# Kernel optimization log

Hardware: AMD Instinct MI355X
Metric: run time of the kernel (lower is better)

The kernel has to match this reference:

```python
import jax, jax.numpy as jnp
import numpy as np

D_INPUT, D_MODEL, D_OUTPUT, D_STATE, FACTOR = 100, 256, 100, 64, 2
N2 = D_STATE // 2  # complex conjugate-pair states (S4D)
B_SZ, L_SEQ = 16, 4096


def setup_inputs() -> dict:
    key = jax.random.key(0)
    ks = jax.random.split(key, 12)
    H, N = D_MODEL, N2
    # S4D ('diag-lin', zoh, real_transform='exp') parameters
    log_dt = jax.random.uniform(ks[0], (H,)) * (np.log(0.1) - np.log(0.001)) + np.log(0.001)
    log_A_real = jnp.log(0.5 * jnp.ones((H, N), jnp.float32))
    A_imag = jnp.pi * jnp.broadcast_to(jnp.arange(N, dtype=jnp.float32), (H, N))
    B_re = jnp.ones((H, N), jnp.float32)
    B_im = jnp.zeros((H, N), jnp.float32)
    C_re = jax.random.normal(ks[1], (H, N), jnp.float32)
    C_im = jax.random.normal(ks[2], (H, N), jnp.float32)
    Dskip = jax.random.normal(ks[3], (H,), jnp.float32)
    return {
        'x': jax.random.normal(ks[4], (B_SZ, L_SEQ, D_INPUT), jnp.float32),
        'enc_w': jax.random.normal(ks[5], (D_MODEL, D_INPUT), jnp.float32) / np.sqrt(D_INPUT),
        'enc_b': jnp.zeros((D_MODEL,), jnp.float32),
        'log_dt': log_dt, 'log_A_real': log_A_real, 'A_imag': A_imag,
        'B_re': B_re, 'B_im': B_im, 'C_re': C_re, 'C_im': C_im, 'Dskip': Dskip,
        'ln_g': jnp.ones((D_MODEL,), jnp.float32),
        'ln_b': jnp.zeros((D_MODEL,), jnp.float32),
        'dec1_w': jax.random.normal(ks[6], (D_MODEL * FACTOR, D_MODEL), jnp.float32) / np.sqrt(D_MODEL),
        'dec1_b': jnp.zeros((D_MODEL * FACTOR,), jnp.float32),
        'dec2_w': jax.random.normal(ks[7], (D_OUTPUT, D_MODEL * FACTOR), jnp.float32) / np.sqrt(D_MODEL * FACTOR),
        'dec2_b': jnp.zeros((D_OUTPUT,), jnp.float32),
    }


def s4d_kernel(log_dt, log_A_real, A_imag, B_re, B_im, C_re, C_im, L):
    # diagonal SSM kernel, ZOH discretization: K[h,l] = 2 Re sum_n C'_hn exp(dt_h A_hn)^l
    dt = jnp.exp(log_dt)[:, None]                      # (H,1)
    A = -jnp.exp(log_A_real) + 1j * A_imag             # (H,N)
    C = (B_re + 1j * B_im) * (C_re + 1j * C_im)        # (H,N), B folded into C
    dtA = dt * A                                       # (H,N)
    C = C * (jnp.exp(dtA) - 1.0) / A                   # ZOH correction
    V = jnp.exp(dtA[:, :, None] * jnp.arange(L))       # (H,N,L) Vandermonde
    return 2.0 * jnp.einsum('hn,hnl->hl', C, V).real   # (H,L)


def reference(x, enc_w, enc_b, log_dt, log_A_real, A_imag, B_re, B_im, C_re, C_im,
              Dskip, ln_g, ln_b, dec1_w, dec1_b, dec2_w, dec2_b):
    B, L, _ = x.shape
    u = (x @ enc_w.T + enc_b).transpose(0, 2, 1)       # (B,H,L)
    # FFTConv (single layer), dropout = identity (eval)
    k = s4d_kernel(log_dt, log_A_real, A_imag, B_re, B_im, C_re, C_im, L)
    n = 2 * L
    y = jnp.fft.irfft(jnp.fft.rfft(u, n=n) * jnp.fft.rfft(k, n=n)[None], n=n)[..., :L]
    y = y + u * Dskip[None, :, None]
    y = jax.nn.gelu(y, approximate=False)
    h = y + u                                          # residual
    # LayerNorm over channel dim
    t = h.transpose(0, 2, 1)                           # (B,L,H)
    mu = t.mean(-1, keepdims=True)
    var = jnp.mean((t - mu) ** 2, axis=-1, keepdims=True)
    t = (t - mu) / jnp.sqrt(var + 1e-5) * ln_g + ln_b
    # decoder MLP
    out = jax.nn.gelu(t @ dec1_w.T + dec1_b, approximate=False) @ dec2_w.T + dec2_b
    return out
```

## Files before the change

kernel.cpp:

```cpp
#include <hip/hip_runtime.h>
#include <hip/hip_bf16.h>

#define BB    16
#define LL    4096
#define DIN   100
#define HD    256
#define NN    32
#define DHID  512
#define DOUT  100
#define MROWS (BB*LL)
#define CH    64
#define CC    64
#define NCH   (BB*CC)

#define OFF_WRE    0
#define OFF_WIM    8192
#define OFF_KRE    16384
#define OFF_KIM    24576
#define OFF_WCHR   32768
#define OFF_WCHI   40960
#define OFF_ENCB   49152
#define OFF_DSK    49408
#define OFF_LNG    49664
#define OFF_LNB    49920
#define OFF_B1     50176
#define OFF_B2     50688
#define OFF_WENCB  50816
#define OFF_W1B    67200
#define OFF_W2B    132736
#define OFF_WFL    165504
#define OFF_BY     1230464
#define OFF_VST    2279040
#define OFF_UH     2803328
#define OFF_S      11191936
#define OFF_YH     19580544
#define OFF_TB     OFF_S
#define OFF_G0     OFF_UH
#define OFF_G1     OFF_YH
#define OFF_XB     OFF_YH

typedef __bf16 bf16x8 __attribute__((ext_vector_type(8)));
typedef float  f32x4  __attribute__((ext_vector_type(4)));

static __device__ __forceinline__ int probe_bf16(const void* lng) {
    return ((const unsigned int*)lng)[0] != 0x3f800000u;
}
static __device__ __forceinline__ float ldin(const void* p, long i, int isbf) {
    return isbf ? __bfloat162float(((const __hip_bfloat16*)p)[i]) : ((const float*)p)[i];
}
static __device__ __forceinline__ unsigned short f2bf(float v) {
    union { float f; unsigned u; } c; c.f = v;
    unsigned r = c.u + 0x7fffu + ((c.u >> 16) & 1u);
    return (unsigned short)(r >> 16);
}
static __device__ __forceinline__ float bf2f(unsigned short v) {
    union { unsigned u; float f; } c; c.u = ((unsigned)v) << 16; return c.f;
}
static __device__ __forceinline__ float gelu_f(float x) {
    float z  = fabsf(x) * 0.70710678118654752f;
    float tt = __builtin_amdgcn_rcpf(fmaf(0.3275911f, z, 1.0f));
    float p  = tt * fmaf(tt, fmaf(tt, fmaf(tt, fmaf(tt, 1.061405429f, -1.453152027f),
                          1.421413741f), -0.284496736f), 0.254829592f);
    float er = 1.0f - p * __expf(-z * z);
    return 0.5f * x * (1.0f + copysignf(er, x));
}
static __device__ __forceinline__ void gl2lds16(const unsigned short* g, unsigned short* l) {
    __builtin_amdgcn_global_load_lds(
        (const __attribute__((address_space(1))) unsigned int*)g,
        (__attribute__((address_space(3))) unsigned int*)l, 16, 0, 0);
}

__global__ __launch_bounds__(256) void k_prep(
    const void* encw, const void* encb, const void* logdt, const void* loga,
    const void* aim, const void* bre, const void* bim, const void* cre,
    const void* cim, const void* dsk, const void* lng, const void* lnb,
    const void* w1, const void* b1, const void* w2, const void* b2, float* ws)
{
    const int isbf = probe_bf16(lng);
    unsigned short* WEB = (unsigned short*)(ws + OFF_WENCB);
    unsigned short* W1B = (unsigned short*)(ws + OFF_W1B);
    unsigned short* W2B = (unsigned short*)(ws + OFF_W2B);
    const int total = 8192 + 256*4 + 512 + 128 + 32768 + 131072 + 65536;
    for (int idx = blockIdx.x * blockDim.x + threadIdx.x; idx < total;
         idx += gridDim.x * blockDim.x) {
        int i = idx;
        if (i < 8192) {
            int h = i >> 5;
            float dt  = expf(ldin(logdt, h, isbf));
            float Are = -expf(ldin(loga, i, isbf));
            float Aim = ldin(aim, i, isbf);
            float er  = expf(dt * Are);
            float sv, cv; sincosf(dt * Aim, &sv, &cv);
            float wre = er * cv, wim = er * sv;
            float Bre = ldin(bre, i, isbf), Bim = ldin(bim, i, isbf);
            float Cre = ldin(cre, i, isbf), Cim = ldin(cim, i, isbf);
            float C0re = Bre*Cre - Bim*Cim;
            float C0im = Bre*Cim + Bim*Cre;
            float inv = 1.0f / (Are*Are + Aim*Aim);
            float nre = wre - 1.0f, nim = wim;
            float Zre = (nre*Are + nim*Aim) * inv;
            float Zim = (nim*Are - nre*Aim) * inv;
            float kre = 2.0f * (C0re*Zre - C0im*Zim);
            float kim = -2.0f * (C0re*Zim + C0im*Zre);
            ws[OFF_WRE + i] = wre;  ws[OFF_WIM + i] = wim;
            ws[OFF_KRE + i] = kre;  ws[OFF_KIM + i] = kim;
            float* Wf = ws + OFF_WFL + (long)h * 4160 + 2*(i & 31);
            float pr = 1.0f, pi = 0.0f;
            for (int d = 0; d <= 64; ++d) {
                Wf[d*64]     = pr;
                Wf[d*64 + 1] = pi;
                float tr = pr*wre - pi*wim;
                pi = pr*wim + pi*wre; pr = tr;
            }
            ws[OFF_WCHR + i] = Wf[64*64];
            ws[OFF_WCHI + i] = Wf[64*64 + 1];
        } else if ((i -= 8192) < 256) {
            ws[OFF_ENCB + i] = ldin(encb, i, isbf);
        } else if ((i -= 256) < 256) {
            ws[OFF_DSK + i] = ldin(dsk, i, isbf);
        } else if ((i -= 256) < 256) {
            ws[OFF_LNG + i] = ldin(lng, i, isbf);
        } else if ((i -= 256) < 256) {
            ws[OFF_LNB + i] = ldin(lnb, i, isbf);
        } else if ((i -= 256) < 512) {
            ws[OFF_B1 + i] = ldin(b1, i, isbf);
        } else if ((i -= 512) < 128) {
            ws[OFF_B2 + i] = (i < 100) ? ldin(b2, i, isbf) : 0.0f;
        } else if ((i -= 128) < 32768) {
            int h = i >> 7, k = i & 127;
            WEB[i] = (k < 100) ? f2bf(ldin(encw, (long)h*100 + k, isbf)) : (unsigned short)0;
        } else if ((i -= 32768) < 131072) {
            W1B[i] = f2bf(ldin(w1, i, isbf));
        } else if ((i -= 131072) < 65536) {
            int j = i >> 9, k = i & 511;
            W2B[i] = (j < 100) ? f2bf(ldin(w2, (long)j*512 + k, isbf)) : (unsigned short)0;
        }
    }
}

__global__ __launch_bounds__(256) void k_xcvt(const void* x, const void* lng, float* ws)
{
    const int isbf = probe_bf16(lng);
    unsigned short* Xb = (unsigned short*)(ws + OFF_XB);
    const int total = 65536 * 16;
    for (int s = blockIdx.x * 256 + threadIdx.x; s < total; s += 1024 * 256) {
        int row = s >> 4, slot = s & 15;
        int k0 = slot * 8;
        unsigned short pk[8];
        if (!isbf) {
            const float* xr = (const float*)x + (long)row * 100;
            if (slot < 12) {
                float4 a = *(const float4*)(xr + k0);
                float4 b = *(const float4*)(xr + k0 + 4);
                pk[0]=f2bf(a.x); pk[1]=f2bf(a.y); pk[2]=f2bf(a.z); pk[3]=f2bf(a.w);
                pk[4]=f2bf(b.x); pk[5]=f2bf(b.y); pk[6]=f2bf(b.z); pk[7]=f2bf(b.w);
            } else if (slot == 12) {
                float4 a = *(const float4*)(xr + 96);
                pk[0]=f2bf(a.x); pk[1]=f2bf(a.y); pk[2]=f2bf(a.z); pk[3]=f2bf(a.w);
                pk[4]=0; pk[5]=0; pk[6]=0; pk[7]=0;
            } else {
                #pragma unroll
                for (int j = 0; j < 8; ++j) pk[j] = 0;
            }
        } else {
            const unsigned short* xr = (const unsigned short*)x + (long)row * 100;
            if (slot < 12) {
                *(uint2*)&pk[0] = *(const uint2*)(xr + k0);
                *(uint2*)&pk[4] = *(const uint2*)(xr + k0 + 4);
            } else if (slot == 12) {
                *(uint2*)&pk[0] = *(const uint2*)(xr + 96);
                pk[4]=0; pk[5]=0; pk[6]=0; pk[7]=0;
            } else {
                #pragma unroll
                for (int j = 0; j < 8; ++j) pk[j] = 0;
            }
        }
        *(float4*)&Xb[(long)row * 128 + k0] = *(const float4*)pk;
    }
}

__global__ __launch_bounds__(256) void k_tker(float* ws)
{
    __shared__ float Wp[65*65];
    __shared__ float kr[32], ki[32], Ks[64];
    int h = blockIdx.x;
    int t = threadIdx.x;
    for (int idx = t; idx < 4160; idx += 256) {
        int d = idx >> 6, c = idx & 63;
        Wp[d*65 + c] = ws[OFF_WFL + (long)h*4160 + idx];
    }
    if (t < 32) kr[t] = ws[OFF_KRE + h*32 + t];
    else if (t < 64) ki[t-32] = ws[OFF_KIM + h*32 + (t-32)];
    __syncthreads();
    if (t < 64) {
        float s = 0.0f;
        #pragma unroll
        for (int n = 0; n < 32; ++n)
            s += kr[n]*Wp[t*65 + 2*n] + ki[n]*Wp[t*65 + 2*n + 1];
        Ks[t] = s;
    }
    __syncthreads();
    unsigned short* BY = (unsigned short*)(ws + OFF_BY) + (long)h*8192;
    for (int idx = t; idx < 8192; idx += 256) {
        int j = idx >> 7, k = idx & 127;
        float v;
        if (k < 64) {
            v = (k <= j) ? Ks[j - k] : 0.0f;
        } else {
            int c = k - 64, n = c >> 1;
            float pr = Wp[(j+1)*65 + 2*n], pi = Wp[(j+1)*65 + 2*n + 1];
            v = ((c & 1) == 0) ? (kr[n]*pr + ki[n]*pi) : (ki[n]*pr - kr[n]*pi);
        }
        BY[idx] = f2bf(v);
    }
    unsigned short* Vst = (unsigned short*)(ws + OFF_VST) + (long)h*4096;
    for (int idx = t; idx < 4096; idx += 256) {
        int comp = idx >> 6, i = idx & 63;
        Vst[idx] = f2bf(Wp[(63 - i)*65 + comp]);
    }
}

__global__ __launch_bounds__(256) void k_encm(float* ws)
{
    __shared__ unsigned short SM[32768];
    unsigned short* Cs = SM;
    const unsigned short* Xb  = (const unsigned short*)(ws + OFF_XB);
    const unsigned short* WEB = (const unsigned short*)(ws + OFF_WENCB);
    int bid = blockIdx.x;
    int rt = bid >> 1, ct = bid & 1;
    long row0 = (long)rt * 128;
    int c0 = ct * 128;
    int t = threadIdx.x;
    int lane = t & 63, wv = t >> 6;
    int wm = (wv & 1) * 64, wn = (wv >> 1) * 64;
    int quad = lane >> 4, mr = lane & 15;
    int swz = lane & 7;
    int sr = t >> 3, sdst = (t & 7) * 8, ssrc = ((t & 7) ^ (sr & 7)) * 8;
    f32x4 acc[4][4] = {};
    #pragma unroll
    for (int it = 0; it < 4; ++it) {
        int r = sr + it * 32;
        gl2lds16(&Xb[(row0 + r) * 128 + ssrc], &SM[r * 64 + sdst]);
        gl2lds16(&WEB[(long)(c0 + r) * 128 + ssrc], &SM[8192 + r * 64 + sdst]);
    }
    __syncthreads();
    #pragma unroll
    for (int kc = 0; kc < 2; ++kc) {
        const unsigned short* As = &SM[(kc & 1) * 16384];
        const unsigned short* Bs = As + 8192;
        if (kc == 0) {
            #pragma unroll
            for (int it = 0; it < 4; ++it) {
                int r = sr + it * 32;
                gl2lds16(&Xb[(row0 + r) * 128 + 64 + ssrc], &SM[16384 + r * 64 + sdst]);
                gl2lds16(&WEB[(long)(c0 + r) * 128 + 64 + ssrc], &SM[24576 + r * 64 + sdst]);
            }
        }
        #pragma unroll
        for (int ks = 0; ks < 64; ks += 32) {
            int co = (((ks >> 3) | quad) ^ swz) * 8;
            bf16x8 af[4], bfr[4];
            #pragma unroll
            for (int i = 0; i < 4; ++i)
                af[i] = *(const bf16x8*)&As[(wm + i*16 + mr)*64 + co];
            #pragma unroll
            for (int j = 0; j < 4; ++j)
                bfr[j] = *(const bf16x8*)&Bs[(wn + j*16 + mr)*64 + co];
            #pragma unroll
            for (int i = 0; i < 4; ++i)
                #pragma unroll
                for (int j = 0; j < 4; ++j)
                    acc[i][j] = __builtin_amdgcn_mfma_f32_16x16x32_bf16(af[i], bfr[j], acc[i][j], 0, 0, 0);
        }
        __syncthreads();
    }
    const float* eb = ws + OFF_ENCB;
    #pragma unroll
    for (int j = 0; j < 4; ++j) {
        int hloc = wn + j*16 + mr;
        float bb = eb[c0 + hloc];
        #pragma unroll
        for (int i = 0; i < 4; ++i) {
            int l0 = wm + i*16 + quad*4;
            unsigned short pk[4];
            #pragma unroll
            for (int reg = 0; reg < 4; ++reg)
                pk[reg] = f2bf(acc[i][j][reg] + bb);
            *(uint2*)&Cs[hloc*136 + l0] = *(uint2*)pk;
        }
    }
    __syncthreads();
    unsigned short* Uh = (unsigned short*)(ws + OFF_UH);
    #pragma unroll
    for (int it = 0; it < 8; ++it) {
        int idx = t + it*256;
        int hh = idx >> 4, f = idx & 15;
        *(float4*)&Uh[(long)(c0 + hh)*65536 + row0 + f*8] = *(const float4*)&Cs[hh*136 + f*8];
    }
}

__global__ __launch_bounds__(256) void k_state(float* ws)
{
    __shared__ unsigned short As[128][72];
    __shared__ unsigned short Bs[64][72];
    const unsigned short* Uh  = (const unsigned short*)(ws + OFF_UH);
    const unsigned short* Vst = (const unsigned short*)(ws + OFF_VST);
    int bid = blockIdx.x;
    int h = bid >> 3, ct = bid & 7;
    int c0r = ct * 128;
    int t = threadIdx.x;
    int lane = t & 63, wv = t >> 6;
    int wm = (wv & 1) * 64, wn = (wv >> 1) * 32;
    int quad = lane >> 4, mr = lane & 15;
    const unsigned short* Ubase = Uh + (long)h * 65536;
    #pragma unroll
    for (int it = 0; it < 4; ++it) {
        int idx = t + it*256;
        int r = idx >> 3, f = idx & 7;
        *(float4*)&As[r][f*8] = *(const float4*)&Ubase[(long)(c0r + r)*64 + f*8];
    }
    #pragma unroll
    for (int it = 0; it < 2; ++it) {
        int idx = t + it*256;
        int r = idx >> 3, f = idx & 7;
        *(float4*)&Bs[r][f*8] = *(const float4*)&Vst[(long)h*4096 + r*64 + f*8];
    }
    __syncthreads();
    f32x4 acc[4][2] = {};
    #pragma unroll
    for (int ks = 0; ks < 64; ks += 32) {
        bf16x8 af[4], bfr[2];
        #pragma unroll
        for (int i = 0; i < 4; ++i)
            af[i] = *(const bf16x8*)&As[wm + i*16 + mr][ks + quad*8];
        #pragma unroll
        for (int jn = 0; jn < 2; ++jn)
            bfr[jn] = *(const bf16x8*)&Bs[wn + jn*16 + mr][ks + quad*8];
        #pragma unroll
        for (int i = 0; i < 4; ++i)
            #pragma unroll
            for (int jn = 0; jn < 2; ++jn)
                acc[i][jn] = __builtin_amdgcn_mfma_f32_16x16x32_bf16(af[i], bfr[jn], acc[i][jn], 0, 0, 0);
    }
    __syncthreads();
    unsigned short* Cs = &As[0][0];
    #pragma unroll
    for (int jn = 0; jn < 2; ++jn) {
        int c = wn + jn*16 + mr;
        #pragma unroll
        for (int i = 0; i < 4; ++i)
            #pragma unroll
            for (int reg = 0; reg < 4; ++reg)
                Cs[(wm + i*16 + quad*4 + reg)*72 + c] = f2bf(acc[i][jn][reg]);
    }
    __syncthreads();
    unsigned short* S = (unsigned short*)(ws + OFF_S);
    #pragma unroll
    for (int it = 0; it < 4; ++it) {
        int idx = t + it*256;
        int r = idx >> 3, f = idx & 7;
        *(float4*)&S[(long)(c0r + r)*16384 + h*64 + f*8] = *(const float4*)&Cs[r*72 + f*8];
    }
}

static __device__ __forceinline__ void chunk_step(unsigned int v, unsigned int* Su,
        long a, float wr, float wi, float& rr, float& ri) {
    float Sr = bf2f((unsigned short)(v & 0xFFFFu));
    float Si = bf2f((unsigned short)(v >> 16));
    Su[a] = (unsigned int)f2bf(rr) | ((unsigned int)f2bf(ri) << 16);
    float nr = fmaf(wr, rr, fmaf(-wi, ri, Sr));
    float ni = fmaf(wr, ri, fmaf(wi, rr, Si));
    rr = nr; ri = ni;
}
__global__ __launch_bounds__(256) void k_chunk(float* ws)
{
    int tid = blockIdx.x * 256 + threadIdx.x;
    int b = tid >> 13;
    int h = (tid >> 5) & 255;
    int n = tid & 31;
    int i = h * NN + n;
    float wr = ws[OFF_WCHR + i], wi = ws[OFF_WCHI + i];
    unsigned int* Su = (unsigned int*)(ws + OFF_S);
    long a0 = (long)(b * CC) * 8192 + h * 32 + n;
    float rr = 0.0f, ri = 0.0f;
    unsigned int v0 = Su[a0];
    unsigned int v1 = Su[a0 + 8192];
    unsigned int v2 = Su[a0 + 2L*8192];
    unsigned int v3 = Su[a0 + 3L*8192];
    for (int c = 0; c < CC; c += 4) {
        long a = a0 + (long)c * 8192;
        unsigned int u0 = v0, u1 = v1, u2 = v2, u3 = v3;
        if (c + 4 < CC) {
            v0 = Su[a + 4L*8192];
            v1 = Su[a + 5L*8192];
            v2 = Su[a + 6L*8192];
            v3 = Su[a + 7L*8192];
        }
        chunk_step(u0, Su, a,           wr, wi, rr, ri);
        chunk_step(u1, Su, a + 8192,    wr, wi, rr, ri);
        chunk_step(u2, Su, a + 2L*8192, wr, wi, rr, ri);
        chunk_step(u3, Su, a + 3L*8192, wr, wi, rr, ri);
    }
}

__global__ __launch_bounds__(256) void k_y(float* ws)
{
    __shared__ unsigned short As[128][136];
    __shared__ unsigned short Bs[64][136];
    const unsigned short* Uh = (const unsigned short*)(ws + OFF_UH);
    const unsigned short* S  = (const unsigned short*)(ws + OFF_S);
    const unsigned short* BY = (const unsigned short*)(ws + OFF_BY);
    int bid = blockIdx.x;
    int h = bid >> 3, ct = bid & 7;
    int c0r = ct * 128;
    int t = threadIdx.x;
    int lane = t & 63, wv = t >> 6;
    int wm = (wv & 1) * 64, wn = (wv >> 1) * 32;
    int quad = lane >> 4, mr = lane & 15;
    #pragma unroll
    for (int it = 0; it < 8; ++it) {
        int idx = t + it*256;
        int r = idx >> 4, f = idx & 15;
        const unsigned short* src = (f < 8)
            ? &Uh[(long)h*65536 + (long)(c0r + r)*64 + f*8]
            : &S[(long)(c0r + r)*16384 + h*64 + (f-8)*8];
        *(float4*)&As[r][f*8] = *(const float4*)src;
    }
    #pragma unroll
    for (int it = 0; it < 4; ++it) {
        int idx = t + it*256;
        int r = idx >> 4, f = idx & 15;
        *(float4*)&Bs[r][f*8] = *(const float4*)&BY[(long)h*8192 + r*128 + f*8];
    }
    __syncthreads();
    f32x4 acc[4][2] = {};
    #pragma unroll
    for (int ks = 0; ks < 128; ks += 32) {
        bf16x8 af[4], bfr[2];
        #pragma unroll
        for (int i = 0; i < 4; ++i)
            af[i] = *(const bf16x8*)&As[wm + i*16 + mr][ks + quad*8];
        #pragma unroll
        for (int jn = 0; jn < 2; ++jn)
            bfr[jn] = *(const bf16x8*)&Bs[wn + jn*16 + mr][ks + quad*8];
        #pragma unroll
        for (int i = 0; i < 4; ++i)
            #pragma unroll
            for (int jn = 0; jn < 2; ++jn)
                acc[i][jn] = __builtin_amdgcn_mfma_f32_16x16x32_bf16(af[i], bfr[jn], acc[i][jn], 0, 0, 0);
    }
    __syncthreads();
    unsigned short* Cs = &As[0][0];
    float Dh = ws[OFF_DSK + h];
    #pragma unroll
    for (int jn = 0; jn < 2; ++jn) {
        int c = wn + jn*16 + mr;
        #pragma unroll
        for (int i = 0; i < 4; ++i)
            #pragma unroll
            for (int reg = 0; reg < 4; ++reg) {
                int row = wm + i*16 + quad*4 + reg;
                float u = bf2f(Cs[row*136 + c]);
                float v = gelu_f(fmaf(Dh, u, acc[i][jn][reg])) + u;
                Cs[row*136 + c] = f2bf(v);
            }
    }
    __syncthreads();
    unsigned short* Vh = (unsigned short*)(ws + OFF_YH);
    #pragma unroll
    for (int it = 0; it < 4; ++it) {
        int idx = t + it*256;
        int r = idx >> 3, f = idx & 7;
        *(float4*)&Vh[(long)h*65536 + (long)(c0r + r)*64 + f*8] = *(const float4*)&Cs[r*136 + f*8];
    }
}

__global__ __launch_bounds__(1024) void k_ln2(float* ws)
{
    __shared__ unsigned short Vs[64][258];
    __shared__ float parts[64][17], partq[64][17];
    __shared__ float Ms[64], Rs[64];
    __shared__ float Gls[256], Bls[256];
    int chunk = blockIdx.x;
    int t = threadIdx.x;
    if (t < 256) { Gls[t] = ws[OFF_LNG + t]; Bls[t] = ws[OFF_LNB + t]; }
    const unsigned short* Vh = (const unsigned short*)(ws + OFF_YH);
    int j = t & 63, hg = t >> 6;
    float ps = 0.0f, pq = 0.0f;
    #pragma unroll 4
    for (int k = 0; k < 16; ++k) {
        int h = hg*16 + k;
        unsigned short raw = Vh[(long)h*65536 + chunk*64 + j];
        float v = bf2f(raw);
        Vs[j][h] = raw;
        ps += v; pq += v*v;
    }
    parts[j][hg] = ps; partq[j][hg] = pq;
    __syncthreads();
    if (t < 64) {
        float s = 0.0f, q = 0.0f;
        #pragma unroll
        for (int g = 0; g < 16; ++g) { s += parts[t][g]; q += partq[t][g]; }
        float mean = s * (1.0f/256.0f);
        float var  = q * (1.0f/256.0f) - mean*mean;
        Ms[t] = mean; Rs[t] = rsqrtf(var + 1e-5f);
    }
    __syncthreads();
    unsigned short* Tb = (unsigned short*)(ws + OFF_TB);
    int h2 = t & 255, jg = t >> 8;
    #pragma unroll 4
    for (int jj = 0; jj < 16; ++jj) {
        int j2 = jg*16 + jj;
        float v = bf2f(Vs[j2][h2]);
        Tb[((long)chunk*64 + j2)*256 + h2] = f2bf((v - Ms[j2]) * Rs[j2] * Gls[h2] + Bls[h2]);
    }
}

__global__ __launch_bounds__(256) void k_dec1m(float* ws)
{
    __shared__ unsigned short SM[16384];
    unsigned short* Cs = SM;
    const unsigned short* Tb  = (const unsigned short*)(ws + OFF_TB);
    const unsigned short* W1B = (const unsigned short*)(ws + OFF_W1B);
    int bid = (blockIdx.x & 7) * 256 + (blockIdx.x >> 3);
    int rt = bid >> 2, ct = bid & 3;
    long row0 = (long)rt * 128;
    int c0 = ct * 128;
    int t = threadIdx.x;
    int lane = t & 63, wv = t >> 6;
    int wm = (wv & 1) * 64, wn = (wv >> 1) * 64;
    int quad = lane >> 4, mr = lane & 15;
    int r1 = t >> 2, c1 = t & 3;
    int r2 = r1 + 64;
    int s1 = (c1 ^ ((r1 & 3) ^ ((r1 >> 2) & 3))) * 8;
    int s2 = (c1 ^ ((r2 & 3) ^ ((r2 >> 2) & 3))) * 8;
    int mrow_a[4], mrow_b[4], coff_a[4], coff_b[4];
    #pragma unroll
    for (int i = 0; i < 4; ++i) {
        int ra = wm + i*16 + mr;
        int rb = wn + i*16 + mr;
        mrow_a[i] = ra * 32; coff_a[i] = (quad ^ ((ra & 3) ^ ((ra >> 2) & 3))) * 8;
        mrow_b[i] = rb * 32; coff_b[i] = (quad ^ ((rb & 3) ^ ((rb >> 2) & 3))) * 8;
    }
    f32x4 acc[4][4] = {};
    gl2lds16(&Tb[(row0 + r1) * 256 + s1], &SM[t * 8]);
    gl2lds16(&Tb[(row0 + r2) * 256 + s2], &SM[2048 + t * 8]);
    gl2lds16(&W1B[(long)(c0 + r1) * 256 + s1], &SM[4096 + t * 8]);
    gl2lds16(&W1B[(long)(c0 + r2) * 256 + s2], &SM[6144 + t * 8]);
    __syncthreads();
    #pragma unroll
    for (int kc = 0; kc < 8; ++kc) {
        const unsigned short* As = &SM[(kc & 1) * 8192];
        const unsigned short* Bs = As + 4096;
        if (kc < 7) {
            int k0 = (kc + 1) * 32;
            unsigned short* D = &SM[((kc + 1) & 1) * 8192];
            gl2lds16(&Tb[(row0 + r1) * 256 + k0 + s1], &D[t * 8]);
            gl2lds16(&Tb[(row0 + r2) * 256 + k0 + s2], &D[2048 + t * 8]);
            gl2lds16(&W1B[(long)(c0 + r1) * 256 + k0 + s1], &D[4096 + t * 8]);
            gl2lds16(&W1B[(long)(c0 + r2) * 256 + k0 + s2], &D[6144 + t * 8]);
        }
        bf16x8 af[4], bfr[4];
        #pragma unroll
        for (int i = 0; i < 4; ++i)
            af[i] = *(const bf16x8*)&As[mrow_a[i] + coff_a[i]];
        #pragma unroll
        for (int j = 0; j < 4; ++j)
            bfr[j] = *(const bf16x8*)&Bs[mrow_b[j] + coff_b[j]];
        #pragma unroll
        for (int i = 0; i < 4; ++i)
            #pragma unroll
            for (int j = 0; j < 4; ++j)
                acc[i][j] = __builtin_amdgcn_mfma_f32_16x16x32_bf16(af[i], bfr[j], acc[i][j], 0, 0, 0);
        __syncthreads();
    }
    const float* b1 = ws + OFF_B1;
    int cswz = quad << 4;
    #pragma unroll
    for (int j = 0; j < 4; ++j) {
        int cloc = wn + j*16 + mr;
        float bb = b1[c0 + cloc];
        int cphys = cloc ^ cswz;
        #pragma unroll
        for (int i = 0; i < 4; ++i)
            #pragma unroll
            for (int reg = 0; reg < 4; ++reg)
                Cs[(wm + i*16 + quad*4 + reg)*128 + cphys] = f2bf(gelu_f(acc[i][j][reg] + bb));
    }
    __syncthreads();
    unsigned short* G = (unsigned short*)(ws + ((ct < 2) ? OFF_G0 : OFF_G1));
    int cl0 = (ct < 2) ? c0 : (c0 - 256);
    #pragma unroll
    for (int it = 0; it < 8; ++it) {
        int idx = t + it*256;
        int r = idx >> 4, f = idx & 15;
        int colp = (f*8) ^ (((r >> 2) & 3) << 4);
        *(float4*)&G[(row0 + r)*256 + cl0 + f*8] = *(const float4*)&Cs[r*128 + colp];
    }
}

__global__ __launch_bounds__(256) void k_dec2m(float* ws, void* out, const void* lng)
{
    const int isbf = probe_bf16(lng);
    __shared__ unsigned short SM[32768];
    unsigned short* Cs = SM;
    const unsigned short* G0  = (const unsigned short*)(ws + OFF_G0);
    const unsigned short* G1  = (const unsigned short*)(ws + OFF_G1);
    const unsigned short* W2B = (const unsigned short*)(ws + OFF_W2B);
    long row0 = (long)blockIdx.x * 128;
    int t = threadIdx.x;
    int lane = t & 63, wv = t >> 6;
    int wm = (wv & 1) * 64, wn = (wv >> 1) * 64;
    int quad = lane >> 4, mr = lane & 15;
    int swz = lane & 7;
    int sr = t >> 3, sdst = (t & 7) * 8, ssrc = ((t & 7) ^ (sr & 7)) * 8;
    f32x4 acc[4][4] = {};
    #pragma unroll
    for (int it = 0; it < 4; ++it) {
        int r = sr + it * 32;
        gl2lds16(&G0[(row0 + r) * 256 + ssrc], &SM[r * 64 + sdst]);
        gl2lds16(&W2B[(long)r * 512 + ssrc], &SM[8192 + r * 64 + sdst]);
    }
    __syncthreads();
    #pragma unroll
    for (int kc = 0; kc < 8; ++kc) {
        const unsigned short* As = &SM[(kc & 1) * 16384];
        const unsigned short* Bs = As + 8192;
        if (kc < 7) {
            int s = kc + 1;
            const unsigned short* Gsrc = (s < 4) ? G0 : G1;
            int kl = (s & 3) * 64;
            int k0 = s * 64;
            unsigned short* Dst = &SM[(s & 1) * 16384];
            #pragma unroll
            for (int it = 0; it < 4; ++it) {
                int r = sr + it * 32;
                gl2lds16(&Gsrc[(row0 + r) * 256 + kl + ssrc], &Dst[r * 64 + sdst]);
                gl2lds16(&W2B[(long)r * 512 + k0 + ssrc], &Dst[8192 + r * 64 + sdst]);
            }
        }
        #pragma unroll
        for (int ks = 0; ks < 64; ks += 32) {
            int co = (((ks >> 3) | quad) ^ swz) * 8;
            bf16x8 af[4], bfr[4];
            #pragma unroll
            for (int i = 0; i < 4; ++i)
                af[i] = *(const bf16x8*)&As[(wm + i*16 + mr)*64 + co];
            #pragma unroll
            for (int j = 0; j < 4; ++j)
                bfr[j] = *(const bf16x8*)&Bs[(wn + j*16 + mr)*64 + co];
            #pragma unroll
            for (int i = 0; i < 4; ++i)
                #pragma unroll
                for (int j = 0; j < 4; ++j)
                    acc[i][j] = __builtin_amdgcn_mfma_f32_16x16x32_bf16(af[i], bfr[j], acc[i][j], 0, 0, 0);
        }
        __syncthreads();
    }
    const float* b2 = ws + OFF_B2;
    if (isbf) {
        #pragma unroll
        for (int j = 0; j < 4; ++j) {
            int cloc = wn + j*16 + mr;
            float bb = b2[cloc];
            #pragma unroll
            for (int i = 0; i < 4; ++i)
                #pragma unroll
                for (int reg = 0; reg < 4; ++reg)
                    Cs[(wm + i*16 + quad*4 + reg)*136 + cloc] = f2bf(acc[i][j][reg] + bb);
        }
        __syncthreads();
        for (int idx = t; idx < 128*25; idx += 256) {
            int r = idx / 25, f = idx % 25;
            uint2* dst = (uint2*)((char*)out + (row0 + r)*200);
            dst[f] = *(const uint2*)&Cs[r*136 + f*4];
        }
    } else {
        #pragma unroll
        for (int j = 0; j < 4; ++j) {
            int col = wn + j*16 + mr;
            if (col < 100) {
                float bb = b2[col];
                #pragma unroll
                for (int i = 0; i < 4; ++i)
                    #pragma unroll
                    for (int reg = 0; reg < 4; ++reg) {
                        long row = row0 + wm + i*16 + quad*4 + reg;
                        ((float*)out)[row * 100 + col] = acc[i][j][reg] + bb;
                    }
            }
        }
    }
}

extern "C" void kernel_launch(void* const* d_in, const int* in_sizes, int n_in,
                              void* d_out, int out_size, void* d_ws, size_t ws_size,
                              hipStream_t stream)
{
    float* ws = (float*)d_ws;
    k_prep<<<512, 256, 0, stream>>>(d_in[1], d_in[2], d_in[3], d_in[4], d_in[5],
                                    d_in[6], d_in[7], d_in[8], d_in[9], d_in[10],
                                    d_in[11], d_in[12], d_in[13], d_in[14],
                                    d_in[15], d_in[16], ws);
    k_xcvt<<<1024, 256, 0, stream>>>(d_in[0], d_in[11], ws);
    k_tker<<<256, 256, 0, stream>>>(ws);
    k_encm<<<1024, 256, 0, stream>>>(ws);
    k_state<<<2048, 256, 0, stream>>>(ws);
    k_chunk<<<512, 256, 0, stream>>>(ws);
    k_y<<<2048, 256, 0, stream>>>(ws);
    k_ln2<<<NCH, 1024, 0, stream>>>(ws);
    k_dec1m<<<2048, 256, 0, stream>>>(ws);
    k_dec2m<<<512, 256, 0, stream>>>(ws, d_out, d_in[11]);
}
```

Baseline: 262.5 us.

## Halve encoder GEMM LDS footprint with 32-wide K chunks and XOR-swizzled output staging

The encoder GEMM kernel now streams K in four 32-wide double-buffered chunks instead of two 64-wide ones, which cuts its shared memory from 64KB to 32KB and should let more blocks run per CU. A new XOR swizzle is applied to the input tiles, and the output staging buffer drops its padded row stride in favour of an XOR-swizzled 128-element stride so it fits in the smaller allocation. In exchange there are more barriers and load issue points per block, and each chunk offers less MFMA work to hide global-to-LDS latency.

```diff
diff --git a/kernel.cpp b/kernel.cpp
--- a/kernel.cpp
+++ b/kernel.cpp
@@ -222,7 +222,7 @@
 
 __global__ __launch_bounds__(256) void k_encm(float* ws)
 {
-    __shared__ unsigned short SM[32768];
+    __shared__ unsigned short SM[16384];
     unsigned short* Cs = SM;
     const unsigned short* Xb  = (const unsigned short*)(ws + OFF_XB);
     const unsigned short* WEB = (const unsigned short*)(ws + OFF_WENCB);
@@ -234,44 +234,48 @@
     int lane = t & 63, wv = t >> 6;
     int wm = (wv & 1) * 64, wn = (wv >> 1) * 64;
     int quad = lane >> 4, mr = lane & 15;
-    int swz = lane & 7;
-    int sr = t >> 3, sdst = (t & 7) * 8, ssrc = ((t & 7) ^ (sr & 7)) * 8;
+    int r1 = t >> 2, c1 = t & 3;
+    int r2 = r1 + 64;
+    int s1 = (c1 ^ ((r1 & 3) ^ ((r1 >> 2) & 3))) * 8;
+    int s2 = (c1 ^ ((r2 & 3) ^ ((r2 >> 2) & 3))) * 8;
+    int mrow_a[4], mrow_b[4], coff_a[4], coff_b[4];
+    #pragma unroll
+    for (int i = 0; i < 4; ++i) {
+        int ra = wm + i*16 + mr;
+        int rb = wn + i*16 + mr;
+        mrow_a[i] = ra * 32; coff_a[i] = (quad ^ ((ra & 3) ^ ((ra >> 2) & 3))) * 8;
+        mrow_b[i] = rb * 32; coff_b[i] = (quad ^ ((rb & 3) ^ ((rb >> 2) & 3))) * 8;
+    }
     f32x4 acc[4][4] = {};
-    #pragma unroll
-    for (int it = 0; it < 4; ++it) {
-        int r = sr + it * 32;
-        gl2lds16(&Xb[(row0 + r) * 128 + ssrc], &SM[r * 64 + sdst]);
-        gl2lds16(&WEB[(long)(c0 + r) * 128 + ssrc], &SM[8192 + r * 64 + sdst]);
-    }
-    __syncthreads();
-    #pragma unroll
-    for (int kc = 0; kc < 2; ++kc) {
-        const unsigned short* As = &SM[(kc & 1) * 16384];
-        const unsigned short* Bs = As + 8192;
-        if (kc == 0) {
-            #pragma unroll
-            for (int it = 0; it < 4; ++it) {
-                int r = sr + it * 32;
-                gl2lds16(&Xb[(row0 + r) * 128 + 64 + ssrc], &SM[16384 + r * 64 + sdst]);
-                gl2lds16(&WEB[(long)(c0 + r) * 128 + 64 + ssrc], &SM[24576 + r * 64 + sdst]);
-            }
-        }
-        #pragma unroll
-        for (int ks = 0; ks < 64; ks += 32) {
-            int co = (((ks >> 3) | quad) ^ swz) * 8;
-            bf16x8 af[4], bfr[4];
-            #pragma unroll
-            for (int i = 0; i < 4; ++i)
-                af[i] = *(const bf16x8*)&As[(wm + i*16 + mr)*64 + co];
+    gl2lds16(&Xb[(row0 + r1) * 128 + s1], &SM[t * 8]);
+    gl2lds16(&Xb[(row0 + r2) * 128 + s2], &SM[2048 + t * 8]);
+    gl2lds16(&WEB[(long)(c0 + r1) * 128 + s1], &SM[4096 + t * 8]);
+    gl2lds16(&WEB[(long)(c0 + r2) * 128 + s2], &SM[6144 + t * 8]);
+    __syncthreads();
+    #pragma unroll
+    for (int kc = 0; kc < 4; ++kc) {
+        const unsigned short* As = &SM[(kc & 1) * 8192];
+        const unsigned short* Bs = As + 4096;
+        if (kc < 3) {
+            int k0 = (kc + 1) * 32;
+            unsigned short* D = &SM[((kc + 1) & 1) * 8192];
+            gl2lds16(&Xb[(row0 + r1) * 128 + k0 + s1], &D[t * 8]);
+            gl2lds16(&Xb[(row0 + r2) * 128 + k0 + s2], &D[2048 + t * 8]);
+            gl2lds16(&WEB[(long)(c0 + r1) * 128 + k0 + s1], &D[4096 + t * 8]);
+            gl2lds16(&WEB[(long)(c0 + r2) * 128 + k0 + s2], &D[6144 + t * 8]);
+        }
+        bf16x8 af[4], bfr[4];
+        #pragma unroll
+        for (int i = 0; i < 4; ++i)
+            af[i] = *(const bf16x8*)&As[mrow_a[i] + coff_a[i]];
+        #pragma unroll
+        for (int j = 0; j < 4; ++j)
+            bfr[j] = *(const bf16x8*)&Bs[mrow_b[j] + coff_b[j]];
+        #pragma unroll
+        for (int i = 0; i < 4; ++i)
             #pragma unroll
             for (int j = 0; j < 4; ++j)
-                bfr[j] = *(const bf16x8*)&Bs[(wn + j*16 + mr)*64 + co];
-            #pragma unroll
-            for (int i = 0; i < 4; ++i)
-                #pragma unroll
-                for (int j = 0; j < 4; ++j)
-                    acc[i][j] = __builtin_amdgcn_mfma_f32_16x16x32_bf16(af[i], bfr[j], acc[i][j], 0, 0, 0);
-        }
+                acc[i][j] = __builtin_amdgcn_mfma_f32_16x16x32_bf16(af[i], bfr[j], acc[i][j], 0, 0, 0);
         __syncthreads();
     }
     const float* eb = ws + OFF_ENCB;
@@ -279,6 +283,7 @@
     for (int j = 0; j < 4; ++j) {
         int hloc = wn + j*16 + mr;
         float bb = eb[c0 + hloc];
+        int hx = (hloc & 7) << 4;
         #pragma unroll
         for (int i = 0; i < 4; ++i) {
             int l0 = wm + i*16 + quad*4;
@@ -286,7 +291,7 @@
             #pragma unroll
             for (int reg = 0; reg < 4; ++reg)
                 pk[reg] = f2bf(acc[i][j][reg] + bb);
-            *(uint2*)&Cs[hloc*136 + l0] = *(uint2*)pk;
+            *(uint2*)&Cs[hloc*128 + (l0 ^ hx)] = *(uint2*)pk;
         }
     }
     __syncthreads();
@@ -295,7 +300,8 @@
     for (int it = 0; it < 8; ++it) {
         int idx = t + it*256;
         int hh = idx >> 4, f = idx & 15;
-        *(float4*)&Uh[(long)(c0 + hh)*65536 + row0 + f*8] = *(const float4*)&Cs[hh*136 + f*8];
+        int colp = (f*8) ^ ((hh & 7) << 4);
+        *(float4*)&Uh[(long)(c0 + hh)*65536 + row0 + f*8] = *(const float4*)&Cs[hh*128 + colp];
     }
 }
 
```

Result: no change. 261.4 us (-0.4%).
